# Optimization experiments

Measured on AMD Instinct MI355X. Metric: run time of the kernel, lower is better.

Reference implementation:

```python
import jax, jax.numpy as jnp
import numpy as np

G = 14       # patch_size
K = 4        # patch_amount
SCALE = 2    # scale_factor (undefined global in source; canonical RAM value)
C = 1
EPS = 1e-5   # torch BatchNorm1d default eps


def extract_patch(x, loc, size):
    # x: (B, C, H, W), loc in [-1, 1]. Always pad (zero-pad is value-equivalent
    # to the source's conditional padding) then gather with dynamic_slice.
    B, C_, H, W = x.shape
    pad = size // 2 + 1
    xp = jnp.pad(x, ((0, 0), (0, 0), (pad, pad), (pad, pad)))
    coords = (0.5 * ((loc + 1.0) * H)).astype(jnp.int32)  # denormalize -> (B,2) [x, y]
    x0 = coords[:, 0] - size // 2 + pad
    y0 = coords[:, 1] - size // 2 + pad

    def slice_one(img, yy, xx):
        return jax.lax.dynamic_slice(img, (0, yy, xx), (C_, size, size))

    return jax.vmap(slice_one)(xp, y0, x0)  # (B, C, size, size)


def foveate(x, loc):
    patches = []
    size = G
    for _ in range(K):
        p = extract_patch(x, loc, size)
        k = size // G
        if k > 1:  # F.avg_pool2d(p, k)
            B, C_, s, _ = p.shape
            p = p.reshape(B, C_, G, k, G, k).mean(axis=(3, 5))
        patches.append(p)
        size = int(SCALE * size)
    phi = jnp.concatenate(patches, axis=1)  # (B, K*C, G, G)
    return phi.reshape(phi.shape[0], -1)    # (B, 784)


def batchnorm(h, gamma, beta):
    # training-mode BatchNorm1d: batch stats, biased variance
    m = h.mean(axis=0)
    v = h.var(axis=0)
    return (h - m) * jax.lax.rsqrt(v + EPS) * gamma + beta


def mlp(h, W1, b1, g1, be1, W2, b2, g2, be2):
    h = jax.nn.relu(batchnorm(h @ W1 + b1, g1, be1))
    return batchnorm(h @ W2 + b2, g2, be2)


def setup_inputs() -> dict:
    key = jax.random.key(0)
    ks = jax.random.split(key, 8)
    B, H = 4096, 128
    x = jax.random.uniform(ks[0], (B, C, H, H), dtype=jnp.float32)
    loc = jax.random.uniform(ks[1], (B, 2), minval=-1.0, maxval=1.0, dtype=jnp.float32)

    def lin(k, fi, fo):
        return jax.random.normal(k, (fi, fo), dtype=jnp.float32) * 0.05

    d = {"x": x, "loc": loc}
    d["what_W1"] = lin(ks[2], 784, 128); d["what_b1"] = jnp.zeros((128,), jnp.float32)
    d["what_g1"] = jnp.ones((128,), jnp.float32); d["what_be1"] = jnp.zeros((128,), jnp.float32)
    d["what_W2"] = lin(ks[3], 128, 256); d["what_b2"] = jnp.zeros((256,), jnp.float32)
    d["what_g2"] = jnp.ones((256,), jnp.float32); d["what_be2"] = jnp.zeros((256,), jnp.float32)
    d["where_W1"] = lin(ks[4], 2, 128); d["where_b1"] = jnp.zeros((128,), jnp.float32)
    d["where_g1"] = jnp.ones((128,), jnp.float32); d["where_be1"] = jnp.zeros((128,), jnp.float32)
    d["where_W2"] = lin(ks[5], 128, 256); d["where_b2"] = jnp.zeros((256,), jnp.float32)
    d["where_g2"] = jnp.ones((256,), jnp.float32); d["where_be2"] = jnp.zeros((256,), jnp.float32)
    return d


def reference(x, loc, what_W1, what_b1, what_g1, what_be1, what_W2, what_b2, what_g2, what_be2, where_W1, where_b1, where_g1, where_be1, where_W2, where_b2, where_g2, where_be2):
    phi = foveate(x, loc)  # (B, 784)
    res_phi = mlp(phi, what_W1, what_b1, what_g1, what_be1, what_W2, what_b2, what_g2, what_be2)
    res_k = mlp(loc, where_W1, where_b1, where_g1, where_be1, where_W2, where_b2, where_g2, where_be2)
    return jax.nn.relu(res_phi + res_k)  # (B, 256)
```

## Files before the change

kernel.cpp:

```cpp
#include <hip/hip_runtime.h>
#include <hip/hip_bf16.h>

typedef __hip_bfloat16 bf16;

static constexpr int kB = 4096;
static constexpr float kEPS = 1e-5f;

__device__ __forceinline__ float cvt(float v) { return v; }
__device__ __forceinline__ float cvt(bf16 v)  { return __bfloat162float(v); }

__device__ __forceinline__ int detect_dtype(const void* __restrict__ x) {
    const bf16* p = (const bf16*)x;
    int isf32 = 0;
    for (int i = 0; i < 64; ++i) {
        float v = __bfloat162float(p[i]);
        if (!(fabsf(v) <= 2.0f)) isf32 = 1;
    }
    return isf32;
}

template <typename T>
__device__ void foveate_impl(const T* __restrict__ x, const T* __restrict__ loc,
                             float* __restrict__ phi, float* __restrict__ L1,
                             float* __restrict__ L2) {
    int b = blockIdx.x;
    float lx = cvt(loc[2 * b + 0]);
    float ly = cvt(loc[2 * b + 1]);
    int cx = (int)(0.5f * ((lx + 1.0f) * 128.0f));
    int cy = (int)(0.5f * ((ly + 1.0f) * 128.0f));
    const T* img = x + (size_t)b * 16384;
    float* ph = phi + (size_t)b * 784;

    int by0 = cy - 56, bx0 = cx - 56;
    for (int i = threadIdx.x; i < 56 * 56; i += 256) {
        int oy = i / 56, ox = i - oy * 56;
        int gy = by0 + 2 * oy, gx = bx0 + 2 * ox;
        float v00 = ((unsigned)gy       < 128u && (unsigned)gx       < 128u) ? cvt(img[gy * 128 + gx])           : 0.f;
        float v01 = ((unsigned)gy       < 128u && (unsigned)(gx + 1) < 128u) ? cvt(img[gy * 128 + gx + 1])       : 0.f;
        float v10 = ((unsigned)(gy + 1) < 128u && (unsigned)gx       < 128u) ? cvt(img[(gy + 1) * 128 + gx])     : 0.f;
        float v11 = ((unsigned)(gy + 1) < 128u && (unsigned)(gx + 1) < 128u) ? cvt(img[(gy + 1) * 128 + gx + 1]) : 0.f;
        L1[oy * 57 + ox] = ((v00 + v01) + v10) + v11;
    }
    __syncthreads();

    for (int i = threadIdx.x; i < 196; i += 256) {
        int r = i / 14, c = i % 14;
        int gy = cy - 7 + r, gx = cx - 7 + c;
        float v = ((unsigned)gy < 128u && (unsigned)gx < 128u) ? cvt(img[gy * 128 + gx]) : 0.f;
        ph[i] = v;
        ph[196 + i] = L1[(21 + r) * 57 + 21 + c] * 0.25f;
    }
    for (int i = threadIdx.x; i < 784; i += 256) {
        int oy = i / 28, ox = i % 28;
        const float* p = L1 + (2 * oy) * 57 + 2 * ox;
        L2[oy * 29 + ox] = p[0] + p[1] + p[57] + p[58];
    }
    __syncthreads();

    for (int i = threadIdx.x; i < 196; i += 256) {
        int r = i / 14, c = i % 14;
        ph[392 + i] = L2[(7 + r) * 29 + 7 + c] * 0.0625f;
        const float* p = L2 + (2 * r) * 29 + 2 * c;
        ph[588 + i] = (p[0] + p[1] + p[29] + p[30]) * 0.015625f;
    }
}

__global__ __launch_bounds__(256) void foveate_kernel(const void* __restrict__ x,
                                                      const void* __restrict__ loc,
                                                      float* __restrict__ phi,
                                                      int* __restrict__ flag) {
    __shared__ float L1[56 * 57];
    __shared__ float L2[28 * 29];
    int isf32 = detect_dtype(x);
    if (blockIdx.x == 0 && threadIdx.x == 0) *flag = isf32;
    if (isf32) foveate_impl<float>((const float*)x, (const float*)loc, phi, L1, L2);
    else       foveate_impl<bf16>((const bf16*)x, (const bf16*)loc, phi, L1, L2);
}

template <typename T>
__device__ void gemm1_impl(const float* __restrict__ A, const T* __restrict__ W,
                           const T* __restrict__ bias, float* __restrict__ C,
                           float* __restrict__ part_s, float* __restrict__ part_q,
                           float* As, float* Bs) {
    int tid = threadIdx.x;
    int tx = tid & 15, ty = tid >> 4;
    int row0 = blockIdx.y * 64, n0 = blockIdx.x * 32;

    float acc[4][2] = {};
    int am = tid >> 2;
    int ak = (tid & 3) << 2;
    int bn = tid & 31;
    int bk = tid >> 5;

    const float* Aptr = A + (size_t)(row0 + am) * 784 + ak;
    float4 av = *(const float4*)Aptr;
    float b0 = cvt(W[(size_t)bk * 128 + n0 + bn]);
    float b1 = cvt(W[(size_t)(bk + 8) * 128 + n0 + bn]);

    for (int t = 0; t < 49; ++t) {
        As[(ak + 0) * 68 + am] = av.x; As[(ak + 1) * 68 + am] = av.y;
        As[(ak + 2) * 68 + am] = av.z; As[(ak + 3) * 68 + am] = av.w;
        Bs[bk * 32 + bn] = b0; Bs[(bk + 8) * 32 + bn] = b1;
        __syncthreads();
        if (t < 48) {
            int k0 = (t + 1) << 4;
            av = *(const float4*)(Aptr + k0);
            b0 = cvt(W[(size_t)(k0 + bk) * 128 + n0 + bn]);
            b1 = cvt(W[(size_t)(k0 + bk + 8) * 128 + n0 + bn]);
        }
#pragma unroll
        for (int k = 0; k < 16; ++k) {
            float4 a  = *(const float4*)&As[k * 68 + ty * 4];
            float2 bb = *(const float2*)&Bs[k * 32 + tx * 2];
            acc[0][0] = fmaf(a.x, bb.x, acc[0][0]); acc[0][1] = fmaf(a.x, bb.y, acc[0][1]);
            acc[1][0] = fmaf(a.y, bb.x, acc[1][0]); acc[1][1] = fmaf(a.y, bb.y, acc[1][1]);
            acc[2][0] = fmaf(a.z, bb.x, acc[2][0]); acc[2][1] = fmaf(a.z, bb.y, acc[2][1]);
            acc[3][0] = fmaf(a.w, bb.x, acc[3][0]); acc[3][1] = fmaf(a.w, bb.y, acc[3][1]);
        }
        __syncthreads();
    }

    float bv0 = cvt(bias[n0 + tx * 2]);
    float bv1 = cvt(bias[n0 + tx * 2 + 1]);
    float cs0 = 0.f, cs1 = 0.f, cq0 = 0.f, cq1 = 0.f;
#pragma unroll
    for (int i = 0; i < 4; ++i) {
        float v0 = acc[i][0] + bv0, v1 = acc[i][1] + bv1;
        float2 o; o.x = v0; o.y = v1;
        *(float2*)(C + (size_t)(row0 + ty * 4 + i) * 128 + n0 + tx * 2) = o;
        cs0 += v0; cq0 += v0 * v0; cs1 += v1; cq1 += v1 * v1;
    }
    __syncthreads();
    As[ty * 32 + tx * 2]     = cs0; As[ty * 32 + tx * 2 + 1] = cs1;
    Bs[ty * 32 + tx * 2]     = cq0; Bs[ty * 32 + tx * 2 + 1] = cq1;
    __syncthreads();
    if (tid < 32) {
        float s = 0.f, q = 0.f;
#pragma unroll
        for (int p = 0; p < 16; ++p) { s += As[p * 32 + tid]; q += Bs[p * 32 + tid]; }
        part_s[(size_t)blockIdx.y * 128 + n0 + tid] = s;
        part_q[(size_t)blockIdx.y * 128 + n0 + tid] = q;
    }
}

__global__ __launch_bounds__(256) void gemm1_fused(const float* __restrict__ A,
                                                   const void* __restrict__ W,
                                                   const void* __restrict__ bias,
                                                   float* __restrict__ C,
                                                   float* __restrict__ part_s,
                                                   float* __restrict__ part_q,
                                                   const int* __restrict__ flag) {
    __shared__ __align__(16) float As[16 * 68];
    __shared__ __align__(16) float Bs[16 * 32];
    if (*flag) gemm1_impl<float>(A, (const float*)W, (const float*)bias, C, part_s, part_q, As, Bs);
    else       gemm1_impl<bf16>(A, (const bf16*)W, (const bf16*)bias, C, part_s, part_q, As, Bs);
}

template <typename T>
__device__ void where1_impl(const T* __restrict__ loc, const T* __restrict__ W,
                            const T* __restrict__ bias, float* __restrict__ q1,
                            float* __restrict__ part_s, float* __restrict__ part_q,
                            float* redS, float* redQ) {
    int c    = threadIdx.x & 127;
    int rsub = threadIdx.x >> 7;
    int rbase = blockIdx.x * 64;
    float w0 = cvt(W[c]), w1 = cvt(W[128 + c]), bv = cvt(bias[c]);
    float s = 0.f, q = 0.f;
#pragma unroll
    for (int p = 0; p < 32; ++p) {
        int r = rbase + rsub + 2 * p;
        float v = fmaf(cvt(loc[2 * r]), w0, fmaf(cvt(loc[2 * r + 1]), w1, bv));
        q1[(size_t)r * 128 + c] = v;
        s += v; q += v * v;
    }
    redS[threadIdx.x] = s; redQ[threadIdx.x] = q;
    __syncthreads();
    if (threadIdx.x < 128) {
        part_s[(size_t)blockIdx.x * 128 + c] = redS[c] + redS[c + 128];
        part_q[(size_t)blockIdx.x * 128 + c] = redQ[c] + redQ[c + 128];
    }
}

__global__ __launch_bounds__(256) void where1_fused(const void* __restrict__ loc,
                                                    const void* __restrict__ W,
                                                    const void* __restrict__ bias,
                                                    float* __restrict__ q1,
                                                    float* __restrict__ part_s,
                                                    float* __restrict__ part_q,
                                                    const int* __restrict__ flag) {
    __shared__ float redS[256], redQ[256];
    if (*flag) where1_impl<float>((const float*)loc, (const float*)W, (const float*)bias, q1, part_s, part_q, redS, redQ);
    else       where1_impl<bf16>((const bf16*)loc, (const bf16*)W, (const bf16*)bias, q1, part_s, part_q, redS, redQ);
}

template <typename T>
__device__ void fin_impl(const float* __restrict__ pS, const float* __restrict__ pQ,
                         const T* __restrict__ g, const T* __restrict__ be,
                         float* __restrict__ st) {
    int c = threadIdx.x;
    double s = 0.0, q = 0.0;
    for (int p = 0; p < 64; ++p) {
        s += (double)pS[p * 128 + c];
        q += (double)pQ[p * 128 + c];
    }
    double mean = s / 4096.0;
    double var  = q / 4096.0 - mean * mean;
    float rstd  = (float)(1.0 / sqrt(var + (double)kEPS));
    float scale = rstd * cvt(g[c]);
    st[c]       = scale;
    st[128 + c] = cvt(be[c]) - (float)mean * scale;
}

__global__ __launch_bounds__(128) void finalize_both(
        const float* __restrict__ pS1, const float* __restrict__ pQ1,
        const void* __restrict__ g1, const void* __restrict__ be1, float* __restrict__ st1,
        const float* __restrict__ pSw1, const float* __restrict__ pQw1,
        const void* __restrict__ gw1, const void* __restrict__ bew1, float* __restrict__ sw1,
        const int* __restrict__ flag) {
    const float* pS = blockIdx.x ? pSw1 : pS1;
    const float* pQ = blockIdx.x ? pQw1 : pQ1;
    const void*  g  = blockIdx.x ? gw1  : g1;
    const void*  be = blockIdx.x ? bew1 : be1;
    float* st       = blockIdx.x ? sw1  : st1;
    if (*flag) fin_impl<float>(pS, pQ, (const float*)g, (const float*)be, st);
    else       fin_impl<bf16>(pS, pQ, (const bf16*)g, (const bf16*)be, st);
}

template <typename T>
__device__ void gemm2_impl(const float* __restrict__ A, const T* __restrict__ W,
                           const T* __restrict__ bias, const float* __restrict__ st,
                           float* __restrict__ C, float* __restrict__ part_s,
                           float* __restrict__ part_q, float* As, float* Bs) {
    int tid = threadIdx.x;
    int tx = tid & 15, ty = tid >> 4;
    int row0 = blockIdx.y * 64, n0 = blockIdx.x * 64;

    float acc[4][4] = {};
    int am = tid >> 2, ak = (tid & 3) << 2;
    int bn = tid & 63, bk0 = tid >> 6;

    const float* Aptr = A + (size_t)(row0 + am) * 128 + ak;
    float4 av = *(const float4*)Aptr;
    float4 sc = *(const float4*)(st + ak);
    float4 sh = *(const float4*)(st + 128 + ak);
    float bv[4];
#pragma unroll
    for (int p = 0; p < 4; ++p) bv[p] = cvt(W[(size_t)(bk0 + 4 * p) * 256 + n0 + bn]);

    for (int t = 0; t < 8; ++t) {
        As[(ak + 0) * 68 + am] = fmaxf(fmaf(av.x, sc.x, sh.x), 0.f);
        As[(ak + 1) * 68 + am] = fmaxf(fmaf(av.y, sc.y, sh.y), 0.f);
        As[(ak + 2) * 68 + am] = fmaxf(fmaf(av.z, sc.z, sh.z), 0.f);
        As[(ak + 3) * 68 + am] = fmaxf(fmaf(av.w, sc.w, sh.w), 0.f);
#pragma unroll
        for (int p = 0; p < 4; ++p) Bs[(bk0 + 4 * p) * 64 + bn] = bv[p];
        __syncthreads();
        if (t < 7) {
            int k0 = (t + 1) << 4;
            av = *(const float4*)(Aptr + k0);
            sc = *(const float4*)(st + k0 + ak);
            sh = *(const float4*)(st + 128 + k0 + ak);
#pragma unroll
            for (int p = 0; p < 4; ++p) bv[p] = cvt(W[(size_t)(k0 + bk0 + 4 * p) * 256 + n0 + bn]);
        }
#pragma unroll
        for (int k = 0; k < 16; ++k) {
            float4 a = *(const float4*)&As[k * 68 + ty * 4];
            float4 b = *(const float4*)&Bs[k * 64 + tx * 4];
            acc[0][0] = fmaf(a.x, b.x, acc[0][0]); acc[0][1] = fmaf(a.x, b.y, acc[0][1]);
            acc[0][2] = fmaf(a.x, b.z, acc[0][2]); acc[0][3] = fmaf(a.x, b.w, acc[0][3]);
            acc[1][0] = fmaf(a.y, b.x, acc[1][0]); acc[1][1] = fmaf(a.y, b.y, acc[1][1]);
            acc[1][2] = fmaf(a.y, b.z, acc[1][2]); acc[1][3] = fmaf(a.y, b.w, acc[1][3]);
            acc[2][0] = fmaf(a.z, b.x, acc[2][0]); acc[2][1] = fmaf(a.z, b.y, acc[2][1]);
            acc[2][2] = fmaf(a.z, b.z, acc[2][2]); acc[2][3] = fmaf(a.z, b.w, acc[2][3]);
            acc[3][0] = fmaf(a.w, b.x, acc[3][0]); acc[3][1] = fmaf(a.w, b.y, acc[3][1]);
            acc[3][2] = fmaf(a.w, b.z, acc[3][2]); acc[3][3] = fmaf(a.w, b.w, acc[3][3]);
        }
        __syncthreads();
    }

    float bb[4];
#pragma unroll
    for (int j = 0; j < 4; ++j) bb[j] = cvt(bias[n0 + tx * 4 + j]);
    float cs[4] = {}, cq[4] = {};
#pragma unroll
    for (int i = 0; i < 4; ++i) {
        float v0 = acc[i][0] + bb[0], v1 = acc[i][1] + bb[1];
        float v2 = acc[i][2] + bb[2], v3 = acc[i][3] + bb[3];
        float4 o; o.x = v0; o.y = v1; o.z = v2; o.w = v3;
        cs[0] += v0; cs[1] += v1; cs[2] += v2; cs[3] += v3;
        cq[0] += v0 * v0; cq[1] += v1 * v1; cq[2] += v2 * v2; cq[3] += v3 * v3;
        *(float4*)(C + (size_t)(row0 + ty * 4 + i) * 256 + n0 + tx * 4) = o;
    }
    __syncthreads();
#pragma unroll
    for (int j = 0; j < 4; ++j) {
        As[ty * 64 + tx * 4 + j] = cs[j];
        Bs[ty * 64 + tx * 4 + j] = cq[j];
    }
    __syncthreads();
    if (tid < 64) {
        float s = 0.f, q = 0.f;
#pragma unroll
        for (int p = 0; p < 16; ++p) { s += As[p * 64 + tid]; q += Bs[p * 64 + tid]; }
        part_s[(size_t)blockIdx.y * 256 + n0 + tid] = s;
        part_q[(size_t)blockIdx.y * 256 + n0 + tid] = q;
    }
}

__global__ __launch_bounds__(256) void gemm23_fused(
        const float* __restrict__ h1, const float* __restrict__ q1,
        const void* __restrict__ wW2, const void* __restrict__ wb2,
        const void* __restrict__ hW2, const void* __restrict__ hb2,
        const float* __restrict__ st1, const float* __restrict__ sw1,
        float* __restrict__ h2, float* __restrict__ q2,
        float* __restrict__ pS2, float* __restrict__ pQ2,
        float* __restrict__ pSw2, float* __restrict__ pQw2,
        const int* __restrict__ flag) {
    __shared__ __align__(16) float As[16 * 68];
    __shared__ __align__(16) float Bs[16 * 64];
    const float* A;  const void* W; const void* bias; const float* st;
    float* C; float* ps; float* pq;
    if (blockIdx.z == 0) { A = h1; W = wW2; bias = wb2; st = st1; C = h2; ps = pS2;  pq = pQ2;  }
    else                 { A = q1; W = hW2; bias = hb2; st = sw1; C = q2; ps = pSw2; pq = pQw2; }
    if (*flag) gemm2_impl<float>(A, (const float*)W, (const float*)bias, st, C, ps, pq, As, Bs);
    else       gemm2_impl<bf16>(A, (const bf16*)W, (const bf16*)bias, st, C, ps, pq, As, Bs);
}

template <typename T>
__device__ void final_impl(const float* __restrict__ h2, const float* __restrict__ q2,
                           const float* __restrict__ pS2, const float* __restrict__ pQ2,
                           const float* __restrict__ pSw2, const float* __restrict__ pQw2,
                           const T* __restrict__ g2, const T* __restrict__ be2,
                           const T* __restrict__ gw2, const T* __restrict__ bew2,
                           T* __restrict__ out) {
    int c = threadIdx.x;
    double s = 0.0, q = 0.0, sw = 0.0, qw = 0.0;
    for (int p = 0; p < 64; ++p) {
        s  += (double)pS2[p * 256 + c];  q  += (double)pQ2[p * 256 + c];
        sw += (double)pSw2[p * 256 + c]; qw += (double)pQw2[p * 256 + c];
    }
    double mH = s / 4096.0,  vH = q / 4096.0 - mH * mH;
    double mQ = sw / 4096.0, vQ = qw / 4096.0 - mQ * mQ;
    float rH = (float)(1.0 / sqrt(vH + (double)kEPS));
    float rQ = (float)(1.0 / sqrt(vQ + (double)kEPS));
    float aH = rH * cvt(g2[c]);  float bH = cvt(be2[c])  - (float)mH * aH;
    float aQ = rQ * cvt(gw2[c]); float bQ = cvt(bew2[c]) - (float)mQ * aQ;

    for (int idx = blockIdx.x * 256 + c; idx < kB * 256; idx += 256 * 256) {
        float v = fmaxf(fmaf(h2[idx], aH, bH) + fmaf(q2[idx], aQ, bQ), 0.f);
        out[idx] = (T)v;
    }
}

__global__ __launch_bounds__(256) void final_kernel(
        const float* __restrict__ h2, const float* __restrict__ q2,
        const float* __restrict__ pS2, const float* __restrict__ pQ2,
        const float* __restrict__ pSw2, const float* __restrict__ pQw2,
        const void* __restrict__ g2, const void* __restrict__ be2,
        const void* __restrict__ gw2, const void* __restrict__ bew2,
        void* __restrict__ out, const int* __restrict__ flag) {
    if (*flag) final_impl<float>(h2, q2, pS2, pQ2, pSw2, pQw2, (const float*)g2, (const float*)be2,
                                 (const float*)gw2, (const float*)bew2, (float*)out);
    else       final_impl<bf16>(h2, q2, pS2, pQ2, pSw2, pQw2, (const bf16*)g2, (const bf16*)be2,
                                (const bf16*)gw2, (const bf16*)bew2, (bf16*)out);
}

extern "C" void kernel_launch(void* const* d_in, const int* in_sizes, int n_in,
                              void* d_out, int out_size, void* d_ws, size_t ws_size,
                              hipStream_t stream) {
    (void)in_sizes; (void)n_in; (void)out_size; (void)ws_size;
    const void* x    = d_in[0];
    const void* loc  = d_in[1];
    const void* wW1  = d_in[2];
    const void* wb1  = d_in[3];
    const void* wg1  = d_in[4];
    const void* wbe1 = d_in[5];
    const void* wW2  = d_in[6];
    const void* wb2  = d_in[7];
    const void* wg2  = d_in[8];
    const void* wbe2 = d_in[9];
    const void* hW1  = d_in[10];
    const void* hb1  = d_in[11];
    const void* hg1  = d_in[12];
    const void* hbe1 = d_in[13];
    const void* hW2  = d_in[14];
    const void* hb2  = d_in[15];
    const void* hg2  = d_in[16];
    const void* hbe2 = d_in[17];

    int*   flag = (int*)d_ws;
    float* ws   = (float*)d_ws + 16;
    float* phi  = ws;
    float* h1   = phi + (size_t)kB * 784;
    float* q1   = h1  + (size_t)kB * 128;
    float* h2   = q1  + (size_t)kB * 128;
    float* q2   = h2  + (size_t)kB * 256;
    float* st1  = q2  + (size_t)kB * 256;
    float* sw1  = st1 + 256;
    float* pS1  = sw1 + 256;
    float* pQ1  = pS1 + 8192;
    float* pSw1 = pQ1 + 8192;
    float* pQw1 = pSw1 + 8192;
    float* pS2  = phi;
    float* pQ2  = pS2 + 16384;
    float* pSw2 = pQ2 + 16384;
    float* pQw2 = pSw2 + 16384;

    foveate_kernel<<<kB, 256, 0, stream>>>(x, loc, phi, flag);

    gemm1_fused<<<dim3(4, 64), 256, 0, stream>>>(phi, wW1, wb1, h1, pS1, pQ1, flag);
    where1_fused<<<64, 256, 0, stream>>>(loc, hW1, hb1, q1, pSw1, pQw1, flag);

    finalize_both<<<2, 128, 0, stream>>>(pS1, pQ1, wg1, wbe1, st1,
                                         pSw1, pQw1, hg1, hbe1, sw1, flag);

    gemm23_fused<<<dim3(4, 64, 2), 256, 0, stream>>>(h1, q1, wW2, wb2, hW2, hb2,
                                                     st1, sw1, h2, q2,
                                                     pS2, pQ2, pSw2, pQw2, flag);

    final_kernel<<<256, 256, 0, stream>>>(h2, q2, pS2, pQ2, pSw2, pQw2,
                                          wg2, wbe2, hg2, hbe2, d_out, flag);
}
```

Measured before the change: 437.2 us.

## Merge gemm1 with where1 and fold BN1 finalize into gemm2 blocks

Combines the what-path first GEMM and the where-path first layer into a single launch by partitioning the block index, and removes the separate finalize kernel by having every gemm2 block recompute the layer-1 BatchNorm scale/shift from partial sums into shared memory. This cuts two kernel launches and their serialization gaps. In exchange, each of the 512 gemm2 blocks redundantly reduces 64x128 partials in double precision before starting its GEMM, which adds per-block latency.

```diff
diff --git a/kernel.cpp b/kernel.cpp
--- a/kernel.cpp
+++ b/kernel.cpp
@@ -81,10 +81,10 @@
 __device__ void gemm1_impl(const float* __restrict__ A, const T* __restrict__ W,
                            const T* __restrict__ bias, float* __restrict__ C,
                            float* __restrict__ part_s, float* __restrict__ part_q,
-                           float* As, float* Bs) {
+                           float* As , float* Bs ,
+                           int row0, int n0, int by) {
     int tid = threadIdx.x;
     int tx = tid & 15, ty = tid >> 4;
-    int row0 = blockIdx.y * 64, n0 = blockIdx.x * 32;
 
     float acc[4][2] = {};
     int am = tid >> 2;
@@ -138,32 +138,19 @@
         float s = 0.f, q = 0.f;
 #pragma unroll
         for (int p = 0; p < 16; ++p) { s += As[p * 32 + tid]; q += Bs[p * 32 + tid]; }
-        part_s[(size_t)blockIdx.y * 128 + n0 + tid] = s;
-        part_q[(size_t)blockIdx.y * 128 + n0 + tid] = q;
-    }
-}
-
-__global__ __launch_bounds__(256) void gemm1_fused(const float* __restrict__ A,
-                                                   const void* __restrict__ W,
-                                                   const void* __restrict__ bias,
-                                                   float* __restrict__ C,
-                                                   float* __restrict__ part_s,
-                                                   float* __restrict__ part_q,
-                                                   const int* __restrict__ flag) {
-    __shared__ __align__(16) float As[16 * 68];
-    __shared__ __align__(16) float Bs[16 * 32];
-    if (*flag) gemm1_impl<float>(A, (const float*)W, (const float*)bias, C, part_s, part_q, As, Bs);
-    else       gemm1_impl<bf16>(A, (const bf16*)W, (const bf16*)bias, C, part_s, part_q, As, Bs);
+        part_s[(size_t)by * 128 + n0 + tid] = s;
+        part_q[(size_t)by * 128 + n0 + tid] = q;
+    }
 }
 
 template <typename T>
 __device__ void where1_impl(const T* __restrict__ loc, const T* __restrict__ W,
                             const T* __restrict__ bias, float* __restrict__ q1,
                             float* __restrict__ part_s, float* __restrict__ part_q,
-                            float* redS, float* redQ) {
+                            float* redS, float* redQ, int wb) {
     int c    = threadIdx.x & 127;
     int rsub = threadIdx.x >> 7;
-    int rbase = blockIdx.x * 64;
+    int rbase = wb * 64;
     float w0 = cvt(W[c]), w1 = cvt(W[128 + c]), bv = cvt(bias[c]);
     float s = 0.f, q = 0.f;
 #pragma unroll
@@ -176,62 +163,61 @@
     redS[threadIdx.x] = s; redQ[threadIdx.x] = q;
     __syncthreads();
     if (threadIdx.x < 128) {
-        part_s[(size_t)blockIdx.x * 128 + c] = redS[c] + redS[c + 128];
-        part_q[(size_t)blockIdx.x * 128 + c] = redQ[c] + redQ[c + 128];
-    }
-}
-
-__global__ __launch_bounds__(256) void where1_fused(const void* __restrict__ loc,
-                                                    const void* __restrict__ W,
-                                                    const void* __restrict__ bias,
-                                                    float* __restrict__ q1,
-                                                    float* __restrict__ part_s,
-                                                    float* __restrict__ part_q,
-                                                    const int* __restrict__ flag) {
-    __shared__ float redS[256], redQ[256];
-    if (*flag) where1_impl<float>((const float*)loc, (const float*)W, (const float*)bias, q1, part_s, part_q, redS, redQ);
-    else       where1_impl<bf16>((const bf16*)loc, (const bf16*)W, (const bf16*)bias, q1, part_s, part_q, redS, redQ);
-}
-
-template <typename T>
-__device__ void fin_impl(const float* __restrict__ pS, const float* __restrict__ pQ,
-                         const T* __restrict__ g, const T* __restrict__ be,
-                         float* __restrict__ st) {
-    int c = threadIdx.x;
-    double s = 0.0, q = 0.0;
-    for (int p = 0; p < 64; ++p) {
-        s += (double)pS[p * 128 + c];
-        q += (double)pQ[p * 128 + c];
-    }
-    double mean = s / 4096.0;
-    double var  = q / 4096.0 - mean * mean;
-    float rstd  = (float)(1.0 / sqrt(var + (double)kEPS));
-    float scale = rstd * cvt(g[c]);
-    st[c]       = scale;
-    st[128 + c] = cvt(be[c]) - (float)mean * scale;
-}
-
-__global__ __launch_bounds__(128) void finalize_both(
-        const float* __restrict__ pS1, const float* __restrict__ pQ1,
-        const void* __restrict__ g1, const void* __restrict__ be1, float* __restrict__ st1,
-        const float* __restrict__ pSw1, const float* __restrict__ pQw1,
-        const void* __restrict__ gw1, const void* __restrict__ bew1, float* __restrict__ sw1,
+        part_s[(size_t)wb * 128 + c] = redS[c] + redS[c + 128];
+        part_q[(size_t)wb * 128 + c] = redQ[c] + redQ[c + 128];
+    }
+}
+
+__global__ __launch_bounds__(256) void gemm1_where1(
+        const float* __restrict__ phi, const void* __restrict__ wW1,
+        const void* __restrict__ wb1, float* __restrict__ h1,
+        float* __restrict__ pS1, float* __restrict__ pQ1,
+        const void* __restrict__ loc, const void* __restrict__ hW1,
+        const void* __restrict__ hb1, float* __restrict__ q1,
+        float* __restrict__ pSw1, float* __restrict__ pQw1,
         const int* __restrict__ flag) {
-    const float* pS = blockIdx.x ? pSw1 : pS1;
-    const float* pQ = blockIdx.x ? pQw1 : pQ1;
-    const void*  g  = blockIdx.x ? gw1  : g1;
-    const void*  be = blockIdx.x ? bew1 : be1;
-    float* st       = blockIdx.x ? sw1  : st1;
-    if (*flag) fin_impl<float>(pS, pQ, (const float*)g, (const float*)be, st);
-    else       fin_impl<bf16>(pS, pQ, (const bf16*)g, (const bf16*)be, st);
+    __shared__ __align__(16) float As[16 * 68];
+    __shared__ __align__(16) float Bs[16 * 32];
+    if (blockIdx.x < 64) {
+        int wb = blockIdx.x;
+        if (*flag) where1_impl<float>((const float*)loc, (const float*)hW1,
+                                      (const float*)hb1, q1, pSw1, pQw1, As, Bs, wb);
+        else       where1_impl<bf16>((const bf16*)loc, (const bf16*)hW1,
+                                     (const bf16*)hb1, q1, pSw1, pQw1, As, Bs, wb);
+    } else {
+        int g = blockIdx.x - 64;
+        int n0 = (g & 3) * 32, by = g >> 2, row0 = by * 64;
+        if (*flag) gemm1_impl<float>(phi, (const float*)wW1, (const float*)wb1,
+                                     h1, pS1, pQ1, As, Bs, row0, n0, by);
+        else       gemm1_impl<bf16>(phi, (const bf16*)wW1, (const bf16*)wb1,
+                                    h1, pS1, pQ1, As, Bs, row0, n0, by);
+    }
 }
 
 template <typename T>
 __device__ void gemm2_impl(const float* __restrict__ A, const T* __restrict__ W,
-                           const T* __restrict__ bias, const float* __restrict__ st,
+                           const T* __restrict__ bias,
+                           const float* __restrict__ pS, const float* __restrict__ pQ,
+                           const T* __restrict__ g1v, const T* __restrict__ be1v,
                            float* __restrict__ C, float* __restrict__ part_s,
-                           float* __restrict__ part_q, float* As, float* Bs) {
+                           float* __restrict__ part_q,
+                           float* As, float* Bs, float* stS) {
     int tid = threadIdx.x;
+    if (tid < 128) {
+        double s = 0.0, q = 0.0;
+        for (int p = 0; p < 64; ++p) {
+            s += (double)pS[p * 128 + tid];
+            q += (double)pQ[p * 128 + tid];
+        }
+        double mean = s / 4096.0;
+        double var  = q / 4096.0 - mean * mean;
+        float rstd  = (float)(1.0 / sqrt(var + (double)kEPS));
+        float scale = rstd * cvt(g1v[tid]);
+        stS[tid]       = scale;
+        stS[128 + tid] = cvt(be1v[tid]) - (float)mean * scale;
+    }
+    __syncthreads();
+
     int tx = tid & 15, ty = tid >> 4;
     int row0 = blockIdx.y * 64, n0 = blockIdx.x * 64;
 
@@ -241,8 +227,8 @@
 
     const float* Aptr = A + (size_t)(row0 + am) * 128 + ak;
     float4 av = *(const float4*)Aptr;
-    float4 sc = *(const float4*)(st + ak);
-    float4 sh = *(const float4*)(st + 128 + ak);
+    float4 sc = *(const float4*)(stS + ak);
+    float4 sh = *(const float4*)(stS + 128 + ak);
     float bv[4];
 #pragma unroll
     for (int p = 0; p < 4; ++p) bv[p] = cvt(W[(size_t)(bk0 + 4 * p) * 256 + n0 + bn]);
@@ -258,8 +244,8 @@
         if (t < 7) {
             int k0 = (t + 1) << 4;
             av = *(const float4*)(Aptr + k0);
-            sc = *(const float4*)(st + k0 + ak);
-            sh = *(const float4*)(st + 128 + k0 + ak);
+            sc = *(const float4*)(stS + k0 + ak);
+            sh = *(const float4*)(stS + 128 + k0 + ak);
 #pragma unroll
             for (int p = 0; p < 4; ++p) bv[p] = cvt(W[(size_t)(k0 + bk0 + 4 * p) * 256 + n0 + bn]);
         }
@@ -312,19 +298,31 @@
         const float* __restrict__ h1, const float* __restrict__ q1,
         const void* __restrict__ wW2, const void* __restrict__ wb2,
         const void* __restrict__ hW2, const void* __restrict__ hb2,
-        const float* __restrict__ st1, const float* __restrict__ sw1,
+        const float* __restrict__ pS1, const float* __restrict__ pQ1,
+        const void* __restrict__ wg1, const void* __restrict__ wbe1,
+        const float* __restrict__ pSw1, const float* __restrict__ pQw1,
+        const void* __restrict__ hg1, const void* __restrict__ hbe1,
         float* __restrict__ h2, float* __restrict__ q2,
         float* __restrict__ pS2, float* __restrict__ pQ2,
         float* __restrict__ pSw2, float* __restrict__ pQw2,
         const int* __restrict__ flag) {
     __shared__ __align__(16) float As[16 * 68];
     __shared__ __align__(16) float Bs[16 * 64];
-    const float* A;  const void* W; const void* bias; const float* st;
+    __shared__ __align__(16) float stS[256];
+    const float* A; const void* W; const void* bias;
+    const float* pS; const float* pQ; const void* g1v; const void* be1v;
     float* C; float* ps; float* pq;
-    if (blockIdx.z == 0) { A = h1; W = wW2; bias = wb2; st = st1; C = h2; ps = pS2;  pq = pQ2;  }
-    else                 { A = q1; W = hW2; bias = hb2; st = sw1; C = q2; ps = pSw2; pq = pQw2; }
-    if (*flag) gemm2_impl<float>(A, (const float*)W, (const float*)bias, st, C, ps, pq, As, Bs);
-    else       gemm2_impl<bf16>(A, (const bf16*)W, (const bf16*)bias, st, C, ps, pq, As, Bs);
+    if (blockIdx.z == 0) {
+        A = h1; W = wW2; bias = wb2; pS = pS1;  pQ = pQ1;  g1v = wg1; be1v = wbe1;
+        C = h2; ps = pS2;  pq = pQ2;
+    } else {
+        A = q1; W = hW2; bias = hb2; pS = pSw1; pQ = pQw1; g1v = hg1; be1v = hbe1;
+        C = q2; ps = pSw2; pq = pQw2;
+    }
+    if (*flag) gemm2_impl<float>(A, (const float*)W, (const float*)bias, pS, pQ,
+                                 (const float*)g1v, (const float*)be1v, C, ps, pq, As, Bs, stS);
+    else       gemm2_impl<bf16>(A, (const bf16*)W, (const bf16*)bias, pS, pQ,
+                                (const bf16*)g1v, (const bf16*)be1v, C, ps, pq, As, Bs, stS);
 }
 
 template <typename T>
@@ -396,9 +394,7 @@
     float* q1   = h1  + (size_t)kB * 128;
     float* h2   = q1  + (size_t)kB * 128;
     float* q2   = h2  + (size_t)kB * 256;
-    float* st1  = q2  + (size_t)kB * 256;
-    float* sw1  = st1 + 256;
-    float* pS1  = sw1 + 256;
+    float* pS1  = q2  + (size_t)kB * 256;
     float* pQ1  = pS1 + 8192;
     float* pSw1 = pQ1 + 8192;
     float* pQw1 = pSw1 + 8192;
@@ -407,17 +403,15 @@
     float* pSw2 = pQ2 + 16384;
     float* pQw2 = pSw2 + 16384;
 
-    foveate_kernel<<<kB, 256, 0, stream>>>(x, loc, phi, flag);
-
-    gemm1_fused<<<dim3(4, 64), 256, 0, stream>>>(phi, wW1, wb1, h1, pS1, pQ1, flag);
-    where1_fused<<<64, 256, 0, stream>>>(loc, hW1, hb1, q1, pSw1, pQw1, flag);
-
-    finalize_both<<<2, 128, 0, stream>>>(pS1, pQ1, wg1, wbe1, st1,
-                                         pSw1, pQw1, hg1, hbe1, sw1, flag);
-
-    gemm23_fused<<<dim3(4, 64, 2), 256, 0, stream>>>(h1, q1, wW2, wb2, hW2, hb2,
-                                                     st1, sw1, h2, q2,
-                                                     pS2, pQ2, pSw2, pQw2, flag);
+    foveate_kernel<<<4096, 256, 0, stream>>>(x, loc, phi, flag);
+
+    gemm1_where1<<<320, 256, 0, stream>>>(phi, wW1, wb1, h1, pS1, pQ1,
+                                          loc, hW1, hb1, q1, pSw1, pQw1, flag);
+
+    gemm23_fused<<<dim3(4, 64, 2), 256, 0, stream>>>(
+        h1, q1, wW2, wb2, hW2, hb2,
+        pS1, pQ1, wg1, wbe1, pSw1, pQw1, hg1, hbe1,
+        h2, q2, pS2, pQ2, pSw2, pQw2, flag);
 
     final_kernel<<<256, 256, 0, stream>>>(h2, q2, pS2, pQ2, pSw2, pQw2,
                                           wg2, wbe2, hg2, hbe2, d_out, flag);
```

Result: faster. 428.6 us (-2.0%).
